# Kernel optimization log

Hardware: AMD Instinct MI355X
Metric: run time of the kernel (lower is better)

## Reference

```python
import jax, jax.numpy as jnp
import numpy as np

WS = 7        # window size
IMG = 56      # input resolution (H = W)
BATCH = 32    # image batch
DIM = 384
HEADS = 12
HEAD_DIM = DIM // HEADS
N = WS * WS                      # tokens per window = 49
NW = (IMG // WS) * (IMG // WS)   # windows per image = 64
B_ = BATCH * NW                  # 2048
TBL = (2 * WS - 1) ** 2          # 169


def _rel_index(ws):
    # standard Swin relative position index, values in [0, (2ws-1)^2)
    coords = np.stack(np.meshgrid(np.arange(ws), np.arange(ws), indexing='ij'))
    coords = coords.reshape(2, -1)                       # (2, N)
    rel = coords[:, :, None] - coords[:, None, :]        # (2, N, N)
    rel = rel.transpose(1, 2, 0).astype(np.int64).copy()
    rel[:, :, 0] += ws - 1
    rel[:, :, 1] += ws - 1
    rel[:, :, 0] *= 2 * ws - 1
    return rel.sum(-1)                                   # (N, N)


def _shift_mask(H, W, ws, shift):
    # shifted-window attention mask, (nW, N, N) with 0 / -100
    img = np.zeros((H, W))
    cnt = 0
    for hs in (slice(0, -ws), slice(-ws, -shift), slice(-shift, None)):
        for wsl in (slice(0, -ws), slice(-ws, -shift), slice(-shift, None)):
            img[hs, wsl] = cnt
            cnt += 1
    win = img.reshape(H // ws, ws, W // ws, ws).transpose(0, 2, 1, 3).reshape(-1, ws * ws)
    diff = win[:, None, :] - win[:, :, None]
    return np.where(diff != 0, -100.0, 0.0).astype(np.float32)


def setup_inputs() -> dict:
    key = jax.random.key(0)
    ks = jax.random.split(key, 7)
    s = 0.02
    return {
        'x': jax.random.normal(ks[0], (B_, N, DIM), jnp.float32),
        'mask': jnp.asarray(_shift_mask(IMG, IMG, WS, WS // 2)),
        'rpe_indices': jnp.asarray(_rel_index(WS)),
        'qkv_w': jax.random.normal(ks[1], (3 * DIM, DIM), jnp.float32) * s,
        'qkv_b': jnp.zeros((3 * DIM,), jnp.float32),
        'proj_w': jax.random.normal(ks[2], (DIM, DIM), jnp.float32) * s,
        'proj_b': jnp.zeros((DIM,), jnp.float32),
        'q_rpe': jax.random.normal(ks[3], (HEADS, HEAD_DIM, TBL), jnp.float32) * s,
        'k_rpe': jax.random.normal(ks[4], (HEADS, HEAD_DIM, TBL), jnp.float32) * s,
        'v_rpe': jax.random.normal(ks[5], (HEADS, TBL, HEAD_DIM), jnp.float32) * s,
    }


def reference(x, mask, rpe_indices, qkv_w, qkv_b, proj_w, proj_b, q_rpe, k_rpe, v_rpe):
    B, n, C = x.shape
    h, hd = q_rpe.shape[0], q_rpe.shape[1]
    scale = hd ** -0.5

    qkv = x @ qkv_w.T + qkv_b                                   # (B, N, 3C)
    qkv = qkv.reshape(B, n, 3, h, hd).transpose(2, 0, 3, 1, 4)   # (3, B, h, N, hd)
    q, k, v = qkv[0] * scale, qkv[1], qkv[2]

    attn = jnp.einsum('bhid,bhjd->bhij', q, k)                   # (B, h, N, N)

    # Contextual q/k bias. The torch code does b_q.flatten(2)[:, :, rpe_indices]
    # with rpe_indices in [0, TBL): gathering from the flattened (N*TBL) axis with
    # indices < TBL selects row 0 of the N axis, i.e. b_q[:, :, 0, rpe_indices].
    # We compute only that row, which is mathematically identical.
    bq0 = jnp.einsum('bhd,hdt->bht', q[:, :, 0], q_rpe)          # (B, h, TBL)
    bk0 = jnp.einsum('bhd,hdt->bht', k[:, :, 0], k_rpe)          # (B, h, TBL)
    attn = attn + (bq0 + bk0)[:, :, rpe_indices]                 # gather -> (B, h, N, N)

    nW = mask.shape[0]
    attn = attn.reshape(B // nW, nW, h, n, n) + mask[None, :, None]
    attn = jax.nn.softmax(attn.reshape(B, h, n, n), axis=-1)

    # contextual v bias: w = v_rpe[:, rpe_indices] -> (h, N, N, hd)
    w = v_rpe[:, rpe_indices.reshape(-1)].reshape(h, n, n, hd)
    r_v = jnp.einsum('bhij,hijd->bihd', attn, w).reshape(B, n, C)

    out = jnp.einsum('bhij,bhjd->bihd', attn, v).reshape(B, n, C) + r_v
    out = out @ proj_w.T + proj_b
    return out, attn
```

## Files before the change

### kernel.cpp

```cpp
#include <hip/hip_runtime.h>


typedef unsigned int u32;
typedef unsigned short u16;
typedef __attribute__((ext_vector_type(8))) short bf16x8;
typedef __attribute__((ext_vector_type(4))) float f32x4;
typedef float f4a __attribute__((ext_vector_type(4), aligned(4)));

#define SCALE 0.17677669529663687f

__device__ __forceinline__ u16 f2b(float f) {
  union { float f; u32 u; } c; c.f = f;
  u32 u = c.u;
  return (u16)((u + 0x7FFFu + ((u >> 16) & 1u)) >> 16);
}
__device__ __forceinline__ float b2f(u16 s) {
  union { float f; u32 u; } c; c.u = ((u32)s) << 16;
  return c.f;
}
__device__ __forceinline__ void async16(void* lds, const void* g) {
  __builtin_amdgcn_global_load_lds(
      (const __attribute__((address_space(1))) u32*)g,
      (__attribute__((address_space(3))) u32*)lds, 16, 0, 0);
}

__global__ __launch_bounds__(256) void k_prep(
    const float* __restrict__ qkv_w, const float* __restrict__ proj_w,
    const float* __restrict__ mask, const int* __restrict__ idx,
    const float* __restrict__ x,
    u16* __restrict__ wqkvb, u16* __restrict__ wprojb, u16* __restrict__ mbi,
    u16* __restrict__ xb) {
  int bx = blockIdx.x, tid = threadIdx.x;
  if (bx < 432) {
    int i = bx * 256 + tid;
    float4 v = ((const float4*)qkv_w)[i];
    ushort4 o; o.x = f2b(v.x); o.y = f2b(v.y); o.z = f2b(v.z); o.w = f2b(v.w);
    ((ushort4*)wqkvb)[i] = o;
  } else if (bx < 576) {
    int i = (bx - 432) * 256 + tid;
    float4 v = ((const float4*)proj_w)[i];
    ushort4 o; o.x = f2b(v.x); o.y = f2b(v.y); o.z = f2b(v.z); o.w = f2b(v.w);
    ((ushort4*)wprojb)[i] = o;
  } else if (bx < 1177) {
    int i = (bx - 576) * 256 + tid;
    if (i < 64 * 2401) {
      int p = i % 2401;
      mbi[i] = (u16)(idx[p] | ((mask[i] != 0.0f) ? 256 : 0));
    }
  } else {
    for (int i = (bx - 1177) * 256 + tid; i < 9633792; i += 2048 * 256) {
      float4 v = ((const float4*)x)[i];
      ushort4 o; o.x = f2b(v.x); o.y = f2b(v.y); o.z = f2b(v.z); o.w = f2b(v.w);
      ((ushort4*)xb)[i] = o;
    }
  }
}

__global__ __launch_bounds__(256) void k_qkv(
    const u16* __restrict__ A, const u16* __restrict__ Bw,
    const float* __restrict__ bias, u16* __restrict__ outq) {
  int bx0 = blockIdx.x;
  int bx = (bx0 & 7) * 882 + (bx0 >> 3);
  int mt = bx / 9, nt = bx - mt * 9;
  size_t m0 = (size_t)mt * 128;
  int n0 = nt * 128;
  int tid = threadIdx.x;
  int w = tid >> 6, l = tid & 63;
  int wm = w >> 1, wn = w & 1;
  int lr = l & 15, lg = l >> 4;
  int rdo = (lg ^ ((lr >> 1) & 3)) << 3;

  __shared__ u16 At[3][4096];
  __shared__ u16 Bt[3][4096];

  f32x4 acc[4][4] = {};
  int row = tid >> 2;
  int c8 = (((tid & 3) ^ ((row >> 1) & 3)) << 3);
  const u16* gA  = A + (m0 + row) * 384 + c8;
  const u16* gA2 = A + (m0 + row + 64) * 384 + c8;
  const u16* gB  = Bw + (size_t)(n0 + row) * 384 + c8;
  const u16* gB2 = Bw + (size_t)(n0 + row + 64) * 384 + c8;

  async16(&At[0][tid * 8], gA);
  async16(&At[0][(256 + tid) * 8], gA2);
  async16(&Bt[0][tid * 8], gB);
  async16(&Bt[0][(256 + tid) * 8], gB2);
  async16(&At[1][tid * 8], gA + 32);
  async16(&At[1][(256 + tid) * 8], gA2 + 32);
  async16(&Bt[1][tid * 8], gB + 32);
  async16(&Bt[1][(256 + tid) * 8], gB2 + 32);

#pragma unroll
  for (int t = 0; t < 12; ++t) {
    int cur = t % 3, pre = (t + 2) % 3;
    int k2 = ((t + 2 < 12) ? (t + 2) : 11) * 32;
    async16(&At[pre][tid * 8], gA + k2);
    async16(&At[pre][(256 + tid) * 8], gA2 + k2);
    async16(&Bt[pre][tid * 8], gB + k2);
    async16(&Bt[pre][(256 + tid) * 8], gB2 + k2);
    asm volatile("s_waitcnt vmcnt(8)" ::: "memory");
    asm volatile("s_barrier" ::: "memory");
    bf16x8 af[4], bfr[4];
#pragma unroll
    for (int mi = 0; mi < 4; ++mi)
      af[mi] = *(const bf16x8*)&At[cur][(wm * 64 + mi * 16 + lr) * 32 + rdo];
#pragma unroll
    for (int ni = 0; ni < 4; ++ni)
      bfr[ni] = *(const bf16x8*)&Bt[cur][(wn * 64 + ni * 16 + lr) * 32 + rdo];
#pragma unroll
    for (int mi = 0; mi < 4; ++mi)
#pragma unroll
      for (int ni = 0; ni < 4; ++ni)
        acc[mi][ni] = __builtin_amdgcn_mfma_f32_16x16x32_bf16(af[mi], bfr[ni], acc[mi][ni], 0, 0, 0);
    asm volatile("s_waitcnt lgkmcnt(0)\n\ts_barrier" ::: "memory");
  }
  asm volatile("s_waitcnt vmcnt(0)" ::: "memory");

  int lgq = l >> 4;
#pragma unroll
  for (int ni = 0; ni < 4; ++ni) {
    int cc = n0 + wn * 64 + ni * 16 + lr;
    float bv = bias[cc];
    float sc = (cc < 384) ? SCALE : 1.0f;
#pragma unroll
    for (int mi = 0; mi < 4; ++mi)
#pragma unroll
      for (int r = 0; r < 4; ++r) {
        size_t rr = m0 + wm * 64 + mi * 16 + lgq * 4 + r;
        outq[rr * 1152 + cc] = f2b((acc[mi][ni][r] + bv) * sc);
      }
  }
}

__global__ __launch_bounds__(256) void k_bqk(
    const u16* __restrict__ qkv, const float* __restrict__ q_rpe,
    const float* __restrict__ k_rpe, float* __restrict__ bqk) {
  int bx = blockIdx.x;
  int mtile = bx / 12, h = bx % 12;
  int b0 = mtile * 64;
  int tid = threadIdx.x;
  int w = tid >> 6, l = tid & 63;
  int lr = l & 15, g = l >> 4;

  __shared__ __align__(16) u16 At[64 * 64];
  __shared__ __align__(16) u16 Bt[192 * 64];

  {
    int m = tid >> 2;
#pragma unroll
    for (int rnd = 0; rnd < 2; ++rnd) {
      int c = (tid & 3) + rnd * 4;
      const u16* src = qkv + (size_t)(b0 + m) * 56448 + h * 32 +
                       ((c < 4) ? c * 8 : 384 + (c - 4) * 8);
      bf16x8 v = *(const bf16x8*)src;
      int byte = (m * 128 + c * 16) ^ ((m & 7) << 4);
      *(bf16x8*)((char*)At + byte) = v;
    }
  }
  if (tid < 192) {
    int t = tid;
#pragma unroll
    for (int c = 0; c < 8; ++c) {
      u16 pk[8];
#pragma unroll
      for (int e = 0; e < 8; ++e) {
        int d = (c & 3) * 8 + e;
        float v = 0.f;
        if (t < 169)
          v = (c < 4) ? q_rpe[(h * 32 + d) * 169 + t]
                      : k_rpe[(h * 32 + d) * 169 + t];
        pk[e] = f2b(v);
      }
      int byte = (t * 128 + c * 16) ^ ((t & 7) << 4);
      *(bf16x8*)((char*)Bt + byte) = *(bf16x8*)pk;
    }
  }
  __syncthreads();

  f32x4 acc[12] = {};
  bf16x8 af[2];
#pragma unroll
  for (int ks = 0; ks < 2; ++ks) {
    int row = w * 16 + lr;
    af[ks] = *(const bf16x8*)((const char*)At +
              ((row * 128 + ks * 64 + g * 16) ^ ((row & 7) << 4)));
  }
#pragma unroll
  for (int nt = 0; nt < 12; ++nt) {
#pragma unroll
    for (int ks = 0; ks < 2; ++ks) {
      int t = nt * 16 + lr;
      bf16x8 bf = *(const bf16x8*)((const char*)Bt +
                   ((t * 128 + ks * 64 + g * 16) ^ ((t & 7) << 4)));
      acc[nt] = __builtin_amdgcn_mfma_f32_16x16x32_bf16(af[ks], bf, acc[nt], 0, 0, 0);
    }
  }
#pragma unroll
  for (int nt = 0; nt < 12; ++nt) {
    int t = nt * 16 + lr;
    if (t < 169) {
#pragma unroll
      for (int r = 0; r < 4; ++r) {
        int b = b0 + w * 16 + g * 4 + r;
        bqk[((size_t)b * 12 + h) * 169 + t] = acc[nt][r];
      }
    }
  }
}

__global__ __launch_bounds__(256) void k_attn(
    const u16* __restrict__ qkv, const float* __restrict__ bqkG,
    const u16* __restrict__ mbi,
    float* __restrict__ attn, u16* __restrict__ o1) {
  int blk0 = blockIdx.x;
  int blk = (blk0 & 7) * 768 + (blk0 >> 3);
  int b = blk / 3, hg = blk % 3;
  int tid = threadIdx.x, w = tid >> 6, l = tid & 63;
  int h = hg * 4 + w;
  int lr = l & 15, g = l >> 4;

  __shared__ __align__(16) char LDSR[32160];
  u16* mbiL = (u16*)LDSR;
  float* bqkL = (float*)(LDSR + 4832);
  char* Uw = LDSR + 7584 + w * 6144;
  char* vt = Uw;
  char* slab = Uw + 4096;
  float* aw = (float*)Uw;

  const u16* qbase = qkv + (size_t)b * 49 * 1152 + h * 32;
  const u16* kbase = qbase + 384;
  const u16* vbase = qbase + 768;

  {
    const u16* mrow = mbi + (size_t)(b & 63) * 2401;
    for (int p = tid; p < 2401; p += 256) mbiL[p] = mrow[p];
  }
  {
    int jr = (l < 49) ? l : 48;
    const u16* vr = vbase + (size_t)jr * 1152;
#pragma unroll
    for (int d0 = 0; d0 < 4; ++d0) {
      uint4 vv = *(const uint4*)(vr + d0 * 8);
      u16 el[8];
      *(uint4*)el = vv;
#pragma unroll
      for (int e = 0; e < 8; ++e) {
        int d = d0 * 8 + e;
        int byte = d * 128 + ((l * 2) ^ ((d & 7) << 4));
        *(u16*)(vt + byte) = el[e];
      }
    }
  }
  {
    const float* bg = bqkG + ((size_t)b * 12 + h) * 169;
#pragma unroll
    for (int t0 = 0; t0 < 192; t0 += 64) {
      int t = t0 + l;
      if (t < 169) bqkL[w * 172 + t] = bg[t];
    }
  }

  bf16x8 qf[4], kf[4];
#pragma unroll
  for (int t = 0; t < 4; ++t) {
    int qi = t * 16 + lr;
    int qir = (qi < 49) ? qi : 48;
    qf[t] = *(const bf16x8*)(qbase + (size_t)qir * 1152 + g * 8);
    kf[t] = *(const bf16x8*)(kbase + (size_t)qir * 1152 + g * 8);
  }

  f32x4 S[4][4] = {};
#pragma unroll
  for (int mt = 0; mt < 4; ++mt)
#pragma unroll
    for (int nt = 0; nt < 4; ++nt)
      S[mt][nt] = __builtin_amdgcn_mfma_f32_16x16x32_bf16(kf[mt], qf[nt], S[mt][nt], 0, 0, 0);

  __syncthreads();

#pragma unroll
  for (int nt = 0; nt < 4; ++nt) {
    int qi = nt * 16 + lr;
#pragma unroll
    for (int mt = 0; mt < 4; ++mt)
#pragma unroll
      for (int r = 0; r < 4; ++r) {
        int kj = mt * 16 + g * 4 + r;
        float s = S[mt][nt][r];
        if (qi < 49 && kj < 49) {
          u16 t = mbiL[qi * 49 + kj];
          s += bqkL[w * 172 + (t & 255)] - 100.f * (float)(t >> 8);
        } else {
          s = -1e9f;
        }
        S[mt][nt][r] = s;
      }
  }

  float rinv[4];
#pragma unroll
  for (int nt = 0; nt < 4; ++nt) {
    float m = -1e30f;
#pragma unroll
    for (int mt = 0; mt < 4; ++mt)
#pragma unroll
      for (int r = 0; r < 4; ++r) m = fmaxf(m, S[mt][nt][r]);
    m = fmaxf(m, __shfl_xor(m, 16, 64));
    m = fmaxf(m, __shfl_xor(m, 32, 64));
    float sum = 0.f;
#pragma unroll
    for (int mt = 0; mt < 4; ++mt)
#pragma unroll
      for (int r = 0; r < 4; ++r) {
        float e = __expf(S[mt][nt][r] - m);
        S[mt][nt][r] = e;
        sum += e;
      }
    sum += __shfl_xor(sum, 16, 64);
    sum += __shfl_xor(sum, 32, 64);
    rinv[nt] = 1.f / sum;
  }

  bf16x8 va[2][2];
#pragma unroll
  for (int ks = 0; ks < 2; ++ks)
#pragma unroll
    for (int mtd = 0; mtd < 2; ++mtd) {
      int d = mtd * 16 + lr;
      int byte = d * 128 + ((ks * 64 + g * 16) ^ ((d & 7) << 4));
      va[ks][mtd] = *(const bf16x8*)(vt + byte);
    }

  f32x4 O[2][4] = {};
  int swz = (lr & 7) << 4;
#pragma unroll
  for (int nt = 0; nt < 4; ++nt) {
#pragma unroll
    for (int mt = 0; mt < 4; ++mt) {
      u32 w0 = (u32)f2b(S[mt][nt][0]) | ((u32)f2b(S[mt][nt][1]) << 16);
      u32 w1 = (u32)f2b(S[mt][nt][2]) | ((u32)f2b(S[mt][nt][3]) << 16);
      int off = (lr * 128 + mt * 32 + g * 8) ^ swz;
      uint2 pk = {w0, w1};
      *(uint2*)(slab + off) = pk;
    }
    bf16x8 pb0 = *(const bf16x8*)(slab + ((lr * 128 + g * 16) ^ swz));
    bf16x8 pb1 = *(const bf16x8*)(slab + ((lr * 128 + 64 + g * 16) ^ swz));
#pragma unroll
    for (int mtd = 0; mtd < 2; ++mtd) {
      O[mtd][nt] = __builtin_amdgcn_mfma_f32_16x16x32_bf16(va[0][mtd], pb0, O[mtd][nt], 0, 0, 0);
      O[mtd][nt] = __builtin_amdgcn_mfma_f32_16x16x32_bf16(va[1][mtd], pb1, O[mtd][nt], 0, 0, 0);
    }
  }

  {
    u16* ob = o1 + (size_t)b * 49 * 384 + h * 32;
#pragma unroll
    for (int nti = 0; nti < 4; ++nti) {
      int i = nti * 16 + lr;
      if (i < 49) {
        float riv = rinv[nti];
#pragma unroll
        for (int mtd = 0; mtd < 2; ++mtd) {
          u32 w0 = (u32)f2b(O[mtd][nti][0] * riv) | ((u32)f2b(O[mtd][nti][1] * riv) << 16);
          u32 w1 = (u32)f2b(O[mtd][nti][2] * riv) | ((u32)f2b(O[mtd][nti][3] * riv) << 16);
          uint2 pk = {w0, w1};
          *(uint2*)&ob[(size_t)i * 384 + mtd * 16 + g * 4] = pk;
        }
      }
    }
  }

  asm volatile("s_waitcnt lgkmcnt(0)" ::: "memory");
  float* ao = attn + (size_t)(b * 12 + h) * 2401;
#pragma unroll
  for (int nt = 0; nt < 4; ++nt) {
    int qi = nt * 16 + lr;
    if (qi < 49) {
      float riv = rinv[nt];
#pragma unroll
      for (int mt = 0; mt < 4; ++mt)
#pragma unroll
        for (int r = 0; r < 4; ++r) {
          int kj = mt * 16 + g * 4 + r;
          if (kj < 49) aw[lr * 49 + kj] = S[mt][nt][r] * riv;
        }
    }
    asm volatile("s_waitcnt lgkmcnt(0)" ::: "memory");
    int lim = (nt < 3) ? 784 : 49;
#pragma unroll
    for (int it = 0; it < 13; ++it) {
      int p = l + it * 64;
      if (p < lim) ao[nt * 784 + p] = aw[p];
    }
    asm volatile("s_waitcnt lgkmcnt(0)" ::: "memory");
  }
}

__global__ __launch_bounds__(256) void k_rv(
    const float* __restrict__ attn, const int* __restrict__ idx,
    const float* __restrict__ v_rpe, u16* __restrict__ o1) {
  int bx = blockIdx.x;
  int bc = bx & 7;
  int hi = bx >> 3;
  int i = hi % 49, h = hi / 49;
  int b0 = bc * 256;
  int tid = threadIdx.x;
  int w = tid >> 6, l = tid & 63;
  int lr = l & 15, g = l >> 4;

  __shared__ __align__(16) u16 wT[32 * 64];

  if (tid < 196) {
    int j = tid >> 2, d0 = (tid & 3) * 8;
    const float* vr = v_rpe + ((size_t)h * 169 + idx[i * 49 + j]) * 32 + d0;
    float4 a = *(const float4*)vr;
    float4 bvv = *(const float4*)(vr + 4);
    float el[8] = {a.x, a.y, a.z, a.w, bvv.x, bvv.y, bvv.z, bvv.w};
#pragma unroll
    for (int e = 0; e < 8; ++e) {
      int d = d0 + e;
      int byte = (d * 128 + j * 2) ^ ((d & 7) << 4);
      *(u16*)((char*)wT + byte) = f2b(el[e]);
    }
  } else {
    int t = tid - 196;
    int j = 49 + (t >> 2), d0 = (t & 3) * 8;
#pragma unroll
    for (int e = 0; e < 8; ++e) {
      int d = d0 + e;
      int byte = (d * 128 + j * 2) ^ ((d & 7) << 4);
      *(u16*)((char*)wT + byte) = 0;
    }
  }
  __syncthreads();

  f32x4 acc[2][4] = {};
#pragma unroll
  for (int ks = 0; ks < 2; ++ks) {
    bf16x8 af[2];
#pragma unroll
    for (int mt = 0; mt < 2; ++mt) {
      int d = mt * 16 + lr;
      int byte = (d * 128 + ks * 64 + g * 16) ^ ((d & 7) << 4);
      af[mt] = *(const bf16x8*)((const char*)wT + byte);
    }
    int j0 = ks * 32 + g * 8;
#pragma unroll
    for (int nt = 0; nt < 4; ++nt) {
      int bl = w * 64 + nt * 16 + lr;
      const float* ar = attn + ((size_t)(b0 + bl) * 12 + h) * 2401 +
                        (size_t)i * 49 + j0;
      f4a v0 = *(const f4a*)ar;
      f4a v1 = *(const f4a*)(ar + 4);
      u16 pk[8];
#pragma unroll
      for (int e = 0; e < 8; ++e) {
        float vv = (e < 4) ? v0[e] : v1[e - 4];
        pk[e] = (j0 + e < 49) ? f2b(vv) : (u16)0;
      }
      bf16x8 bfr = *(bf16x8*)pk;
#pragma unroll
      for (int mt = 0; mt < 2; ++mt)
        acc[mt][nt] = __builtin_amdgcn_mfma_f32_16x16x32_bf16(af[mt], bfr, acc[mt][nt], 0, 0, 0);
    }
  }

#pragma unroll
  for (int nt = 0; nt < 4; ++nt) {
    int bl = w * 64 + nt * 16 + lr;
    u16* ob = o1 + ((size_t)(b0 + bl) * 49 + i) * 384 + h * 32;
#pragma unroll
    for (int mt = 0; mt < 2; ++mt) {
      int d = mt * 16 + g * 4;
      uint2 old = *(uint2*)&ob[d];
      uint2 nw;
      nw.x = (u32)f2b(b2f((u16)(old.x & 0xffff)) + acc[mt][nt][0]) |
             ((u32)f2b(b2f((u16)(old.x >> 16)) + acc[mt][nt][1]) << 16);
      nw.y = (u32)f2b(b2f((u16)(old.y & 0xffff)) + acc[mt][nt][2]) |
             ((u32)f2b(b2f((u16)(old.y >> 16)) + acc[mt][nt][3]) << 16);
      *(uint2*)&ob[d] = nw;
    }
  }
}

__global__ __launch_bounds__(256) void k_proj(
    const u16* __restrict__ A, const u16* __restrict__ Bw,
    const float* __restrict__ bias, float* __restrict__ out) {
  int bx0 = blockIdx.x;
  int bx = (bx0 & 7) * 294 + (bx0 >> 3);
  int mt = bx / 3, nt = bx - mt * 3;
  size_t m0 = (size_t)mt * 128;
  int n0 = nt * 128;
  int tid = threadIdx.x;
  int w = tid >> 6, l = tid & 63;
  int wm = w >> 1, wn = w & 1;
  int lr = l & 15, lg = l >> 4;
  int rdo = (lg ^ ((lr >> 1) & 3)) << 3;

  __shared__ u16 At[3][4096];
  __shared__ u16 Bt[3][4096];

  f32x4 acc[4][4] = {};
  int row = tid >> 2;
  int c8 = (((tid & 3) ^ ((row >> 1) & 3)) << 3);
  const u16* gA  = A + (m0 + row) * 384 + c8;
  const u16* gA2 = A + (m0 + row + 64) * 384 + c8;
  const u16* gB  = Bw + (size_t)(n0 + row) * 384 + c8;
  const u16* gB2 = Bw + (size_t)(n0 + row + 64) * 384 + c8;

  async16(&At[0][tid * 8], gA);
  async16(&At[0][(256 + tid) * 8], gA2);
  async16(&Bt[0][tid * 8], gB);
  async16(&Bt[0][(256 + tid) * 8], gB2);
  async16(&At[1][tid * 8], gA + 32);
  async16(&At[1][(256 + tid) * 8], gA2 + 32);
  async16(&Bt[1][tid * 8], gB + 32);
  async16(&Bt[1][(256 + tid) * 8], gB2 + 32);

#pragma unroll
  for (int t = 0; t < 12; ++t) {
    int cur = t % 3, pre = (t + 2) % 3;
    int k2 = ((t + 2 < 12) ? (t + 2) : 11) * 32;
    async16(&At[pre][tid * 8], gA + k2);
    async16(&At[pre][(256 + tid) * 8], gA2 + k2);
    async16(&Bt[pre][tid * 8], gB + k2);
    async16(&Bt[pre][(256 + tid) * 8], gB2 + k2);
    asm volatile("s_waitcnt vmcnt(8)" ::: "memory");
    asm volatile("s_barrier" ::: "memory");
    bf16x8 af[4], bfr[4];
#pragma unroll
    for (int mi = 0; mi < 4; ++mi)
      af[mi] = *(const bf16x8*)&At[cur][(wm * 64 + mi * 16 + lr) * 32 + rdo];
#pragma unroll
    for (int ni = 0; ni < 4; ++ni)
      bfr[ni] = *(const bf16x8*)&Bt[cur][(wn * 64 + ni * 16 + lr) * 32 + rdo];
#pragma unroll
    for (int mi = 0; mi < 4; ++mi)
#pragma unroll
      for (int ni = 0; ni < 4; ++ni)
        acc[mi][ni] = __builtin_amdgcn_mfma_f32_16x16x32_bf16(af[mi], bfr[ni], acc[mi][ni], 0, 0, 0);
    asm volatile("s_waitcnt lgkmcnt(0)\n\ts_barrier" ::: "memory");
  }
  asm volatile("s_waitcnt vmcnt(0)" ::: "memory");

  int lgq = l >> 4;
#pragma unroll
  for (int mi = 0; mi < 4; ++mi)
#pragma unroll
    for (int ni = 0; ni < 4; ++ni)
#pragma unroll
      for (int r = 0; r < 4; ++r) {
        int rr = wm * 64 + mi * 16 + lgq * 4 + r;
        int cc = wn * 64 + ni * 16 + lr;
        out[(m0 + rr) * 384 + (size_t)(n0 + cc)] = acc[mi][ni][r] + bias[n0 + cc];
      }
}

extern "C" void kernel_launch(void* const* d_in, const int* in_sizes, int n_in,
                              void* d_out, int out_size, void* d_ws, size_t ws_size,
                              hipStream_t stream) {
  const float* x      = (const float*)d_in[0];
  const float* mask   = (const float*)d_in[1];
  const int*   rpe    = (const int*)d_in[2];
  const float* qkv_w  = (const float*)d_in[3];
  const float* qkv_b  = (const float*)d_in[4];
  const float* proj_w = (const float*)d_in[5];
  const float* proj_b = (const float*)d_in[6];
  const float* q_rpe  = (const float*)d_in[7];
  const float* k_rpe  = (const float*)d_in[8];
  const float* v_rpe  = (const float*)d_in[9];

  float* out  = (float*)d_out;
  float* attn = out + (size_t)100352 * 384;

  char* ws = (char*)d_ws;
  u16*   qkvb   = (u16*)ws;
  u16*   wqkvb  = (u16*)(ws + 231211008);
  u16*   wprojb = (u16*)(ws + 232095744);
  u16*   mbi    = (u16*)(ws + 232390656);
  float* bqkG   = (float*)(ws + 232697984);
  u16*   xb     = (u16*)(ws + 249311360);
  u16*   o1     = xb;

  k_prep<<<3225, 256, 0, stream>>>(qkv_w, proj_w, mask, rpe, x, wqkvb, wprojb, mbi, xb);
  k_qkv<<<7056, 256, 0, stream>>>(xb, wqkvb, qkv_b, qkvb);
  k_bqk<<<384, 256, 0, stream>>>(qkvb, q_rpe, k_rpe, bqkG);
  k_attn<<<6144, 256, 0, stream>>>(qkvb, bqkG, mbi, attn, o1);
  k_rv<<<4704, 256, 0, stream>>>(attn, rpe, v_rpe, o1);
  k_proj<<<2352, 256, 0, stream>>>(o1, wprojb, proj_b, out);
}
```

Baseline: 579.2 us.

## Store attention probabilities directly from registers, use hardware bf16 conversion, add MFMA priority

Result: slower. 594.2 us (+2.6%).

```diff
diff --git a/kernel.cpp b/kernel.cpp
--- a/kernel.cpp
+++ b/kernel.cpp
@@ -1,4 +1,5 @@
 #include <hip/hip_runtime.h>
+#include <hip/hip_bf16.h>
 
 
 typedef unsigned int u32;
@@ -10,13 +11,14 @@
 #define SCALE 0.17677669529663687f
 
 __device__ __forceinline__ u16 f2b(float f) {
-  union { float f; u32 u; } c; c.f = f;
-  u32 u = c.u;
-  return (u16)((u + 0x7FFFu + ((u >> 16) & 1u)) >> 16);
+  return __bfloat16_as_ushort(__float2bfloat16(f));
 }
 __device__ __forceinline__ float b2f(u16 s) {
   union { float f; u32 u; } c; c.u = ((u32)s) << 16;
   return c.f;
+}
+__device__ __forceinline__ u32 pk2(float lo, float hi) {
+  return (u32)f2b(lo) | ((u32)f2b(hi) << 16);
 }
 __device__ __forceinline__ void async16(void* lds, const void* g) {
   __builtin_amdgcn_global_load_lds(
@@ -225,7 +227,6 @@
   char* Uw = LDSR + 7584 + w * 6144;
   char* vt = Uw;
   char* slab = Uw + 4096;
-  float* aw = (float*)Uw;
 
   const u16* qbase = qkv + (size_t)b * 49 * 1152 + h * 32;
   const u16* kbase = qbase + 384;
@@ -270,11 +271,13 @@
   }
 
   f32x4 S[4][4] = {};
+  __builtin_amdgcn_s_setprio(1);
 #pragma unroll
   for (int mt = 0; mt < 4; ++mt)
 #pragma unroll
     for (int nt = 0; nt < 4; ++nt)
       S[mt][nt] = __builtin_amdgcn_mfma_f32_16x16x32_bf16(kf[mt], qf[nt], S[mt][nt], 0, 0, 0);
+  __builtin_amdgcn_s_setprio(0);
 
   __syncthreads();
 
@@ -337,19 +340,21 @@
   for (int nt = 0; nt < 4; ++nt) {
 #pragma unroll
     for (int mt = 0; mt < 4; ++mt) {
-      u32 w0 = (u32)f2b(S[mt][nt][0]) | ((u32)f2b(S[mt][nt][1]) << 16);
-      u32 w1 = (u32)f2b(S[mt][nt][2]) | ((u32)f2b(S[mt][nt][3]) << 16);
+      u32 w0 = pk2(S[mt][nt][0], S[mt][nt][1]);
+      u32 w1 = pk2(S[mt][nt][2], S[mt][nt][3]);
       int off = (lr * 128 + mt * 32 + g * 8) ^ swz;
       uint2 pk = {w0, w1};
       *(uint2*)(slab + off) = pk;
     }
     bf16x8 pb0 = *(const bf16x8*)(slab + ((lr * 128 + g * 16) ^ swz));
     bf16x8 pb1 = *(const bf16x8*)(slab + ((lr * 128 + 64 + g * 16) ^ swz));
+    __builtin_amdgcn_s_setprio(1);
 #pragma unroll
     for (int mtd = 0; mtd < 2; ++mtd) {
       O[mtd][nt] = __builtin_amdgcn_mfma_f32_16x16x32_bf16(va[0][mtd], pb0, O[mtd][nt], 0, 0, 0);
       O[mtd][nt] = __builtin_amdgcn_mfma_f32_16x16x32_bf16(va[1][mtd], pb1, O[mtd][nt], 0, 0, 0);
     }
+    __builtin_amdgcn_s_setprio(0);
   }
 
   {
@@ -361,8 +366,8 @@
         float riv = rinv[nti];
 #pragma unroll
         for (int mtd = 0; mtd < 2; ++mtd) {
-          u32 w0 = (u32)f2b(O[mtd][nti][0] * riv) | ((u32)f2b(O[mtd][nti][1] * riv) << 16);
-          u32 w1 = (u32)f2b(O[mtd][nti][2] * riv) | ((u32)f2b(O[mtd][nti][3] * riv) << 16);
+          u32 w0 = pk2(O[mtd][nti][0] * riv, O[mtd][nti][1] * riv);
+          u32 w1 = pk2(O[mtd][nti][2] * riv, O[mtd][nti][3] * riv);
           uint2 pk = {w0, w1};
           *(uint2*)&ob[(size_t)i * 384 + mtd * 16 + g * 4] = pk;
         }
@@ -370,29 +375,25 @@
     }
   }
 
-  asm volatile("s_waitcnt lgkmcnt(0)" ::: "memory");
-  float* ao = attn + (size_t)(b * 12 + h) * 2401;
-#pragma unroll
-  for (int nt = 0; nt < 4; ++nt) {
-    int qi = nt * 16 + lr;
-    if (qi < 49) {
-      float riv = rinv[nt];
-#pragma unroll
-      for (int mt = 0; mt < 4; ++mt)
-#pragma unroll
-        for (int r = 0; r < 4; ++r) {
-          int kj = mt * 16 + g * 4 + r;
-          if (kj < 49) aw[lr * 49 + kj] = S[mt][nt][r] * riv;
+  {
+    float* ao = attn + (size_t)(b * 12 + h) * 2401;
+#pragma unroll
+    for (int nt = 0; nt < 4; ++nt) {
+      int qi = nt * 16 + lr;
+      if (qi < 49) {
+        float riv = rinv[nt];
+#pragma unroll
+        for (int mt = 0; mt < 3; ++mt) {
+          f4a st;
+          st[0] = S[mt][nt][0] * riv;
+          st[1] = S[mt][nt][1] * riv;
+          st[2] = S[mt][nt][2] * riv;
+          st[3] = S[mt][nt][3] * riv;
+          *(f4a*)(ao + qi * 49 + mt * 16 + g * 4) = st;
         }
-    }
-    asm volatile("s_waitcnt lgkmcnt(0)" ::: "memory");
-    int lim = (nt < 3) ? 784 : 49;
-#pragma unroll
-    for (int it = 0; it < 13; ++it) {
-      int p = l + it * 64;
-      if (p < lim) ao[nt * 784 + p] = aw[p];
-    }
-    asm volatile("s_waitcnt lgkmcnt(0)" ::: "memory");
+        if (g == 0) ao[qi * 49 + 48] = S[3][nt][0] * riv;
+      }
+    }
   }
 }
 
@@ -452,13 +453,12 @@
                         (size_t)i * 49 + j0;
       f4a v0 = *(const f4a*)ar;
       f4a v1 = *(const f4a*)(ar + 4);
-      u16 pk[8];
-#pragma unroll
-      for (int e = 0; e < 8; ++e) {
-        float vv = (e < 4) ? v0[e] : v1[e - 4];
-        pk[e] = (j0 + e < 49) ? f2b(vv) : (u16)0;
-      }
-      bf16x8 bfr = *(bf16x8*)pk;
+      u32 wd[4];
+      wd[0] = pk2(v0[0], (j0 + 1 < 49) ? v0[1] : 0.f);
+      wd[1] = pk2((j0 + 2 < 49) ? v0[2] : 0.f, (j0 + 3 < 49) ? v0[3] : 0.f);
+      wd[2] = pk2((j0 + 4 < 49) ? v1[0] : 0.f, (j0 + 5 < 49) ? v1[1] : 0.f);
+      wd[3] = pk2((j0 + 6 < 49) ? v1[2] : 0.f, (j0 + 7 < 49) ? v1[3] : 0.f);
+      bf16x8 bfr = *(bf16x8*)wd;
 #pragma unroll
       for (int mt = 0; mt < 2; ++mt)
         acc[mt][nt] = __builtin_amdgcn_mfma_f32_16x16x32_bf16(af[mt], bfr, acc[mt][nt], 0, 0, 0);
@@ -474,10 +474,10 @@
       int d = mt * 16 + g * 4;
       uint2 old = *(uint2*)&ob[d];
       uint2 nw;
-      nw.x = (u32)f2b(b2f((u16)(old.x & 0xffff)) + acc[mt][nt][0]) |
-             ((u32)f2b(b2f((u16)(old.x >> 16)) + acc[mt][nt][1]) << 16);
-      nw.y = (u32)f2b(b2f((u16)(old.y & 0xffff)) + acc[mt][nt][2]) |
-             ((u32)f2b(b2f((u16)(old.y >> 16)) + acc[mt][nt][3]) << 16);
+      nw.x = pk2(b2f((u16)(old.x & 0xffff)) + acc[mt][nt][0],
+                 b2f((u16)(old.x >> 16)) + acc[mt][nt][1]);
+      nw.y = pk2(b2f((u16)(old.y & 0xffff)) + acc[mt][nt][2],
+                 b2f((u16)(old.y >> 16)) + acc[mt][nt][3]);
       *(uint2*)&ob[d] = nw;
     }
   }
```
